# Performance work log

Hardware: AMD Instinct MI355X
Metric: run time of the kernel (lower is better)

The kernel has to match this reference:

```python
import jax, jax.numpy as jnp
import numpy as np

B, A, D, K = 262144, 10, 10, 32  # batch, aspects, aspect dim (=10), projection dim


def setup_inputs() -> dict:
    key = jax.random.key(0)
    ks = jax.random.split(key, 7)
    scale = 0.01
    return {
        "user_rep": jax.random.normal(ks[0], (B, A, D), jnp.float32),
        "item_rep": jax.random.normal(ks[1], (B, A, D), jnp.float32),
        "affinity_matrix": jax.random.uniform(ks[2], (D, D), jnp.float32, -scale, scale),
        "user_projection": jax.random.uniform(ks[3], (K, D), jnp.float32, -scale, scale),
        "user_parameters": jax.random.uniform(ks[4], (K, 1), jnp.float32, -scale, scale),
        "item_projection": jax.random.uniform(ks[5], (K, D), jnp.float32, -scale, scale),
        "item_parameters": jax.random.uniform(ks[6], (K, 1), jnp.float32, -scale, scale),
    }


def reference(user_rep, item_rep, affinity_matrix, user_projection,
              user_parameters, item_projection, item_parameters):
    # affinity: relu( U @ M @ V^T )  -> [B, Au, Av]
    aff = jax.nn.relu(jnp.einsum('bud,de,bve->buv', user_rep, affinity_matrix, item_rep))

    h_user = jnp.einsum('kd,bud->bku', user_projection, user_rep)  # [B,K,Au]
    h_item = jnp.einsum('kd,bvd->bkv', item_projection, item_rep)  # [B,K,Av]

    # user importance branch
    hu = jax.nn.relu(h_user + jnp.einsum('bkv,buv->bku', h_item, aff))
    u_score = jnp.einsum('k,bku->bu', user_parameters[:, 0], hu)   # [B,Au]
    user_asp_importance = jax.nn.softmax(u_score, axis=1)

    # item importance branch
    hi = jax.nn.relu(h_item + jnp.einsum('bku,buv->bkv', h_user, aff))
    i_score = jnp.einsum('k,bkv->bv', item_parameters[:, 0], hi)   # [B,Av]
    item_asp_importance = jax.nn.softmax(i_score, axis=1)

    return (user_asp_importance, item_asp_importance)
```

## Files before the change

kernel.cpp:

```cpp
#include <hip/hip_runtime.h>

#define NB 262144
#define AA 10
#define DD 10
#define KK 32

typedef float v2f __attribute__((ext_vector_type(2)));

static __device__ __forceinline__ float b2f(unsigned short h) {
    union { unsigned u; float f; } c; c.u = ((unsigned)h) << 16; return c.f;
}
static __device__ __forceinline__ float bflo(unsigned w) {
    union { unsigned u; float f; } c; c.u = w << 16; return c.f;
}
static __device__ __forceinline__ float bfhi(unsigned w) {
    union { unsigned u; float f; } c; c.u = w & 0xffff0000u; return c.f;
}
static __device__ __forceinline__ v2f mk2(float a, float b) {
    v2f r; r.x = a; r.y = b; return r;
}

__device__ __forceinline__ int detect_f32(const unsigned short* p, int nshorts,
                                          unsigned expthr, int lane) {
    int bad = 0;
    if (lane < nshorts) {
        unsigned e = (p[lane] >> 7) & 0xFFu;
        bad = (e >= expthr);
    }
    return __any(bad);
}

__global__ __launch_bounds__(64) void prep_weights(
    const unsigned short* __restrict__ wM,
    const unsigned short* __restrict__ wPu,
    const unsigned short* __restrict__ wpu,
    const unsigned short* __restrict__ wPi,
    const unsigned short* __restrict__ wpi,
    float* __restrict__ wf)
{
    const int t = threadIdx.x;
    int f = 0;
    f |= detect_f32(wM,  64, 125, t) << 0;
    f |= detect_f32(wPu, 64, 125, t) << 1;
    f |= detect_f32(wpu, 32, 125, t) << 2;
    f |= detect_f32(wPi, 64, 125, t) << 3;
    f |= detect_f32(wpi, 32, 125, t) << 4;
    const float* fM  = (const float*)wM;
    const float* fPu = (const float*)wPu;
    const float* fpu = (const float*)wpu;
    const float* fPi = (const float*)wPi;
    const float* fpi = (const float*)wpi;
    for (int i = t; i < 100; i += 64) wf[i]       = (f & 1)  ? fM[i]  : b2f(wM[i]);
    for (int i = t; i < 320; i += 64) wf[100 + i] = (f & 2)  ? fPu[i] : b2f(wPu[i]);
    if (t < 32)                       wf[420 + t] = (f & 4)  ? fpu[t] : b2f(wpu[t]);
    for (int i = t; i < 320; i += 64) wf[452 + i] = (f & 8)  ? fPi[i] : b2f(wPi[i]);
    if (t < 32)                       wf[772 + t] = (f & 16) ? fpi[t] : b2f(wpi[t]);
}

__global__ __launch_bounds__(64, 2) void aie_main(
    const unsigned short* __restrict__ user_rep,
    const unsigned short* __restrict__ item_rep,
    const float* __restrict__ wf,
    float* __restrict__ out)
{
    __shared__ float obuf[1408];
    const int t = threadIdx.x;
    const long long b = (long long)blockIdx.x * 64 + t;

    const int fu = detect_f32(user_rep, 64, 137, t);
    const int fi = detect_f32(item_rep, 64, 137, t);

    v2f U2[AA][5], V2[AA][5];

    if (fi) {
        const float4* g = (const float4*)((const float*)item_rep + b * 100);
        #pragma unroll
        for (int j = 0; j < 25; j++) {
            float4 w = g[j];
            int p = 2 * j;
            V2[p / 5][p % 5]             = mk2(w.x, w.y);
            V2[(p + 1) / 5][(p + 1) % 5] = mk2(w.z, w.w);
        }
    } else {
        const uint2* g = (const uint2*)(item_rep + b * 100);
        #pragma unroll
        for (int j = 0; j < 25; j++) {
            uint2 w = g[j];
            int p = 2 * j;
            V2[p / 5][p % 5]             = mk2(bflo(w.x), bfhi(w.x));
            V2[(p + 1) / 5][(p + 1) % 5] = mk2(bflo(w.y), bfhi(w.y));
        }
    }
    if (fu) {
        const float4* g = (const float4*)((const float*)user_rep + b * 100);
        #pragma unroll
        for (int j = 0; j < 25; j++) {
            float4 w = g[j];
            int p = 2 * j;
            U2[p / 5][p % 5]             = mk2(w.x, w.y);
            U2[(p + 1) / 5][(p + 1) % 5] = mk2(w.z, w.w);
        }
    } else {
        const uint2* g = (const uint2*)(user_rep + b * 100);
        #pragma unroll
        for (int j = 0; j < 25; j++) {
            uint2 w = g[j];
            int p = 2 * j;
            U2[p / 5][p % 5]             = mk2(bflo(w.x), bfhi(w.x));
            U2[(p + 1) / 5][(p + 1) % 5] = mk2(bflo(w.y), bfhi(w.y));
        }
    }

    const v2f*  M2  = (const v2f*)wf;
    const v2f*  Pu2 = (const v2f*)(wf + 100);
    const float* pu = wf + 420;
    const v2f*  Pi2 = (const v2f*)(wf + 452);
    const float* pi = wf + 772;

    #pragma unroll
    for (int u = 0; u < AA; u++) {
        v2f um2[5];
        {
            const float x0 = U2[u][0].x;
            #pragma unroll
            for (int j = 0; j < 5; j++) um2[j] = x0 * M2[j];
        }
        #pragma unroll
        for (int d = 1; d < DD; d++) {
            const float x = (d & 1) ? U2[u][d >> 1].y : U2[u][d >> 1].x;
            #pragma unroll
            for (int j = 0; j < 5; j++) um2[j] += x * M2[d * 5 + j];
        }
        v2f Wr2[5];
        #pragma unroll
        for (int j = 0; j < 5; j++) Wr2[j] = mk2(0.f, 0.f);
        #pragma unroll
        for (int v = 0; v < AA; v++) {
            v2f r2 = um2[0] * V2[v][0];
            #pragma unroll
            for (int j = 1; j < 5; j++) r2 += um2[j] * V2[v][j];
            const float r = fmaxf(r2.x + r2.y, 0.f);
            #pragma unroll
            for (int j = 0; j < 5; j++) Wr2[j] += r * V2[v][j];
        }
        float acc = 0.f;
        #pragma unroll 1
        for (int k0 = 0; k0 < KK; k0 += 8) {
            #pragma unroll
            for (int kk = 0; kk < 8; kk++) {
                const int k = k0 + kk;
                v2f a2 = Pu2[k * 5] * U2[u][0];
                v2f c2 = Pi2[k * 5] * Wr2[0];
                #pragma unroll
                for (int j = 1; j < 5; j++) {
                    a2 += Pu2[k * 5 + j] * U2[u][j];
                    c2 += Pi2[k * 5 + j] * Wr2[j];
                }
                const v2f s2 = a2 + c2;
                acc += pu[k] * fmaxf(s2.x + s2.y, 0.f);
            }
        }
        obuf[11 * t + u] = acc;
    }

    #pragma unroll
    for (int v = 0; v < AA; v++) {
        v2f mv2[5];
        #pragma unroll
        for (int dp = 0; dp < 5; dp++) {
            v2f s0 = M2[(2 * dp) * 5]     * V2[v][0];
            v2f s1 = M2[(2 * dp + 1) * 5] * V2[v][0];
            #pragma unroll
            for (int j = 1; j < 5; j++) {
                s0 += M2[(2 * dp) * 5 + j]     * V2[v][j];
                s1 += M2[(2 * dp + 1) * 5 + j] * V2[v][j];
            }
            mv2[dp] = mk2(s0.x + s0.y, s1.x + s1.y);
        }
        v2f Xr2[5];
        #pragma unroll
        for (int j = 0; j < 5; j++) Xr2[j] = mk2(0.f, 0.f);
        #pragma unroll
        for (int u = 0; u < AA; u++) {
            v2f r2 = mv2[0] * U2[u][0];
            #pragma unroll
            for (int j = 1; j < 5; j++) r2 += mv2[j] * U2[u][j];
            const float r = fmaxf(r2.x + r2.y, 0.f);
            #pragma unroll
            for (int j = 0; j < 5; j++) Xr2[j] += r * U2[u][j];
        }
        float acc = 0.f;
        #pragma unroll 1
        for (int k0 = 0; k0 < KK; k0 += 8) {
            #pragma unroll
            for (int kk = 0; kk < 8; kk++) {
                const int k = k0 + kk;
                v2f a2 = Pi2[k * 5] * V2[v][0];
                v2f c2 = Pu2[k * 5] * Xr2[0];
                #pragma unroll
                for (int j = 1; j < 5; j++) {
                    a2 += Pi2[k * 5 + j] * V2[v][j];
                    c2 += Pu2[k * 5 + j] * Xr2[j];
                }
                const v2f s2 = a2 + c2;
                acc += pi[k] * fmaxf(s2.x + s2.y, 0.f);
            }
        }
        obuf[704 + 11 * t + v] = acc;
    }

    #pragma unroll
    for (int h = 0; h < 2; h++) {
        const int base = 704 * h + 11 * t;
        float s[AA];
        #pragma unroll
        for (int u = 0; u < AA; u++) s[u] = obuf[base + u];
        float mx = s[0];
        #pragma unroll
        for (int u = 1; u < AA; u++) mx = fmaxf(mx, s[u]);
        float sum = 0.f;
        #pragma unroll
        for (int u = 0; u < AA; u++) { s[u] = __expf(s[u] - mx); sum += s[u]; }
        const float inv = 1.f / sum;
        #pragma unroll
        for (int u = 0; u < AA; u++) obuf[base + u] = s[u] * inv;
    }
    __syncthreads();

    {
        float2* o0 = (float2*)(out + (size_t)blockIdx.x * 640);
        float2* o1 = (float2*)(out + (size_t)NB * 10 + (size_t)blockIdx.x * 640);
        #pragma unroll
        for (int j = 0; j < 5; j++) {
            int m = t + 64 * j;
            int i = m / 5;
            int u = 2 * (m - 5 * i);
            o0[m] = make_float2(obuf[11 * i + u],       obuf[11 * i + u + 1]);
            o1[m] = make_float2(obuf[704 + 11 * i + u], obuf[704 + 11 * i + u + 1]);
        }
    }
}

extern "C" void kernel_launch(void* const* d_in, const int* in_sizes, int n_in,
                              void* d_out, int out_size, void* d_ws, size_t ws_size,
                              hipStream_t stream) {
    const unsigned short* user_rep = (const unsigned short*)d_in[0];
    const unsigned short* item_rep = (const unsigned short*)d_in[1];
    float* wf = (float*)d_ws;

    hipLaunchKernelGGL(prep_weights, dim3(1), dim3(64), 0, stream,
                       (const unsigned short*)d_in[2], (const unsigned short*)d_in[3],
                       (const unsigned short*)d_in[4], (const unsigned short*)d_in[5],
                       (const unsigned short*)d_in[6], wf);

    hipLaunchKernelGGL(aie_main, dim3(NB / 64), dim3(64), 0, stream,
                       user_rep, item_rep, wf, (float*)d_out);
}
```

Before: 320.1 us.

## Interchange projection loops to k-outer with packed FMA and LDS-stashed intermediates

Restructures both importance branches so the K projection loop is outermost and loops over all 10 aspects inside it. Each k's interleaved weight row is then loaded once, as a uniform scalar operand, and reused across aspects. Weights are repacked in the prep kernel into per-k 24-float rows, and the arithmetic is written as inline-asm v_pk_fma/v_pk_mul with SGPR operands. The affinity-weighted vectors are stashed in per-thread LDS and item_rep is reloaded from global to limit register pressure. Outputs are written directly per thread, which drops the shared-memory transpose and __syncthreads but gives less coalesced stores and adds an extra global read.

```diff
diff --git a/kernel.cpp b/kernel.cpp
--- a/kernel.cpp
+++ b/kernel.cpp
@@ -7,6 +7,25 @@
 
 typedef float v2f __attribute__((ext_vector_type(2)));
 
+static __device__ __forceinline__ v2f mk2(float a, float b) {
+    v2f r; r.x = a; r.y = b; return r;
+}
+static __device__ __forceinline__ v2f pk_fma(v2f a, v2f b, v2f c) {
+    v2f d; asm("v_pk_fma_f32 %0, %1, %2, %3" : "=v"(d) : "v"(a), "v"(b), "v"(c)); return d;
+}
+static __device__ __forceinline__ v2f pk_fma_s(v2f sa, v2f b, v2f c) {
+    v2f d; asm("v_pk_fma_f32 %0, %1, %2, %3" : "=v"(d) : "s"(sa), "v"(b), "v"(c)); return d;
+}
+static __device__ __forceinline__ v2f pk_mul(v2f a, v2f b) {
+    v2f d; asm("v_pk_mul_f32 %0, %1, %2" : "=v"(d) : "v"(a), "v"(b)); return d;
+}
+static __device__ __forceinline__ v2f pk_mul_s(v2f sa, v2f b) {
+    v2f d; asm("v_pk_mul_f32 %0, %1, %2" : "=v"(d) : "s"(sa), "v"(b)); return d;
+}
+static __device__ __forceinline__ v2f pk_add(v2f a, v2f b) {
+    v2f d; asm("v_pk_add_f32 %0, %1, %2" : "=v"(d) : "v"(a), "v"(b)); return d;
+}
+
 static __device__ __forceinline__ float b2f(unsigned short h) {
     union { unsigned u; float f; } c; c.u = ((unsigned)h) << 16; return c.f;
 }
@@ -15,9 +34,6 @@
 }
 static __device__ __forceinline__ float bfhi(unsigned w) {
     union { unsigned u; float f; } c; c.u = w & 0xffff0000u; return c.f;
-}
-static __device__ __forceinline__ v2f mk2(float a, float b) {
-    v2f r; r.x = a; r.y = b; return r;
 }
 
 __device__ __forceinline__ int detect_f32(const unsigned short* p, int nshorts,
@@ -50,11 +66,48 @@
     const float* fpu = (const float*)wpu;
     const float* fPi = (const float*)wPi;
     const float* fpi = (const float*)wpi;
-    for (int i = t; i < 100; i += 64) wf[i]       = (f & 1)  ? fM[i]  : b2f(wM[i]);
-    for (int i = t; i < 320; i += 64) wf[100 + i] = (f & 2)  ? fPu[i] : b2f(wPu[i]);
-    if (t < 32)                       wf[420 + t] = (f & 4)  ? fpu[t] : b2f(wpu[t]);
-    for (int i = t; i < 320; i += 64) wf[452 + i] = (f & 8)  ? fPi[i] : b2f(wPi[i]);
-    if (t < 32)                       wf[772 + t] = (f & 16) ? fpi[t] : b2f(wpi[t]);
+
+    for (int i = t; i < 100; i += 64) wf[i] = (f & 1) ? fM[i] : b2f(wM[i]);
+
+    for (int i = t; i < KK * 24; i += 64) {
+        const int k = i / 24, j = i % 24;
+        float vu = 0.f, vi = 0.f;
+        if (j < 10) {
+            vu = (f & 2) ? fPu[k * 10 + j] : b2f(wPu[k * 10 + j]);
+            vi = (f & 8) ? fPi[k * 10 + j] : b2f(wPi[k * 10 + j]);
+        } else if (j < 20) {
+            vu = (f & 8) ? fPi[k * 10 + j - 10] : b2f(wPi[k * 10 + j - 10]);
+            vi = (f & 2) ? fPu[k * 10 + j - 10] : b2f(wPu[k * 10 + j - 10]);
+        } else if (j == 20) {
+            vu = (f & 4)  ? fpu[k] : b2f(wpu[k]);
+            vi = (f & 16) ? fpi[k] : b2f(wpi[k]);
+        }
+        wf[128 + i] = vu;
+        wf[896 + i] = vi;
+    }
+}
+
+static __device__ __forceinline__ void load_rep(const unsigned short* __restrict__ p,
+                                                int isf32, long long b, v2f R[AA][5]) {
+    if (isf32) {
+        const float4* g = (const float4*)((const float*)p + b * 100);
+        #pragma unroll
+        for (int j = 0; j < 25; j++) {
+            float4 w = g[j];
+            int e = 2 * j;
+            R[e / 5][e % 5]             = mk2(w.x, w.y);
+            R[(e + 1) / 5][(e + 1) % 5] = mk2(w.z, w.w);
+        }
+    } else {
+        const uint2* g = (const uint2*)(p + b * 100);
+        #pragma unroll
+        for (int j = 0; j < 25; j++) {
+            uint2 w = g[j];
+            int e = 2 * j;
+            R[e / 5][e % 5]             = mk2(bflo(w.x), bfhi(w.x));
+            R[(e + 1) / 5][(e + 1) % 5] = mk2(bflo(w.y), bfhi(w.y));
+        }
+    }
 }
 
 __global__ __launch_bounds__(64, 2) void aie_main(
@@ -63,181 +116,167 @@
     const float* __restrict__ wf,
     float* __restrict__ out)
 {
-    __shared__ float obuf[1408];
+    __shared__ v2f stash[64 * 51];
     const int t = threadIdx.x;
     const long long b = (long long)blockIdx.x * 64 + t;
+    v2f* my = &stash[t * 51];
 
     const int fu = detect_f32(user_rep, 64, 137, t);
     const int fi = detect_f32(item_rep, 64, 137, t);
 
     v2f U2[AA][5], V2[AA][5];
-
-    if (fi) {
-        const float4* g = (const float4*)((const float*)item_rep + b * 100);
-        #pragma unroll
-        for (int j = 0; j < 25; j++) {
-            float4 w = g[j];
-            int p = 2 * j;
-            V2[p / 5][p % 5]             = mk2(w.x, w.y);
-            V2[(p + 1) / 5][(p + 1) % 5] = mk2(w.z, w.w);
-        }
-    } else {
-        const uint2* g = (const uint2*)(item_rep + b * 100);
-        #pragma unroll
-        for (int j = 0; j < 25; j++) {
-            uint2 w = g[j];
-            int p = 2 * j;
-            V2[p / 5][p % 5]             = mk2(bflo(w.x), bfhi(w.x));
-            V2[(p + 1) / 5][(p + 1) % 5] = mk2(bflo(w.y), bfhi(w.y));
-        }
-    }
-    if (fu) {
-        const float4* g = (const float4*)((const float*)user_rep + b * 100);
-        #pragma unroll
-        for (int j = 0; j < 25; j++) {
-            float4 w = g[j];
-            int p = 2 * j;
-            U2[p / 5][p % 5]             = mk2(w.x, w.y);
-            U2[(p + 1) / 5][(p + 1) % 5] = mk2(w.z, w.w);
-        }
-    } else {
-        const uint2* g = (const uint2*)(user_rep + b * 100);
-        #pragma unroll
-        for (int j = 0; j < 25; j++) {
-            uint2 w = g[j];
-            int p = 2 * j;
-            U2[p / 5][p % 5]             = mk2(bflo(w.x), bfhi(w.x));
-            U2[(p + 1) / 5][(p + 1) % 5] = mk2(bflo(w.y), bfhi(w.y));
-        }
-    }
-
-    const v2f*  M2  = (const v2f*)wf;
-    const v2f*  Pu2 = (const v2f*)(wf + 100);
-    const float* pu = wf + 420;
-    const v2f*  Pi2 = (const v2f*)(wf + 452);
-    const float* pi = wf + 772;
+    load_rep(item_rep, fi, b, V2);
+    load_rep(user_rep, fu, b, U2);
+
+    const v2f* M2 = (const v2f*)wf;
 
     #pragma unroll
     for (int u = 0; u < AA; u++) {
         v2f um2[5];
         {
-            const float x0 = U2[u][0].x;
-            #pragma unroll
-            for (int j = 0; j < 5; j++) um2[j] = x0 * M2[j];
+            v2f xs = mk2(U2[u][0].x, U2[u][0].x);
+            #pragma unroll
+            for (int j = 0; j < 5; j++) um2[j] = pk_mul_s(M2[j], xs);
         }
         #pragma unroll
         for (int d = 1; d < DD; d++) {
             const float x = (d & 1) ? U2[u][d >> 1].y : U2[u][d >> 1].x;
-            #pragma unroll
-            for (int j = 0; j < 5; j++) um2[j] += x * M2[d * 5 + j];
-        }
-        v2f Wr2[5];
-        #pragma unroll
-        for (int j = 0; j < 5; j++) Wr2[j] = mk2(0.f, 0.f);
+            v2f xs = mk2(x, x);
+            #pragma unroll
+            for (int j = 0; j < 5; j++) um2[j] = pk_fma_s(M2[d * 5 + j], xs, um2[j]);
+        }
+        v2f Wr[5];
+        #pragma unroll
+        for (int j = 0; j < 5; j++) Wr[j] = mk2(0.f, 0.f);
         #pragma unroll
         for (int v = 0; v < AA; v++) {
-            v2f r2 = um2[0] * V2[v][0];
-            #pragma unroll
-            for (int j = 1; j < 5; j++) r2 += um2[j] * V2[v][j];
+            v2f r2 = pk_mul(um2[0], V2[v][0]);
+            #pragma unroll
+            for (int j = 1; j < 5; j++) r2 = pk_fma(um2[j], V2[v][j], r2);
             const float r = fmaxf(r2.x + r2.y, 0.f);
-            #pragma unroll
-            for (int j = 0; j < 5; j++) Wr2[j] += r * V2[v][j];
-        }
-        float acc = 0.f;
-        #pragma unroll 1
-        for (int k0 = 0; k0 < KK; k0 += 8) {
-            #pragma unroll
-            for (int kk = 0; kk < 8; kk++) {
-                const int k = k0 + kk;
-                v2f a2 = Pu2[k * 5] * U2[u][0];
-                v2f c2 = Pi2[k * 5] * Wr2[0];
-                #pragma unroll
-                for (int j = 1; j < 5; j++) {
-                    a2 += Pu2[k * 5 + j] * U2[u][j];
-                    c2 += Pi2[k * 5 + j] * Wr2[j];
-                }
-                const v2f s2 = a2 + c2;
-                acc += pu[k] * fmaxf(s2.x + s2.y, 0.f);
+            v2f rs = mk2(r, r);
+            #pragma unroll
+            for (int j = 0; j < 5; j++) Wr[j] = pk_fma(rs, V2[v][j], Wr[j]);
+        }
+        #pragma unroll
+        for (int j = 0; j < 5; j++) my[u * 5 + j] = Wr[j];
+    }
+    asm volatile("" ::: "memory");
+
+    v2f Wf[AA][5];
+    #pragma unroll
+    for (int u = 0; u < AA; u++)
+        #pragma unroll
+        for (int j = 0; j < 5; j++) Wf[u][j] = my[u * 5 + j];
+
+    float us[AA];
+    #pragma unroll
+    for (int u = 0; u < AA; u++) us[u] = 0.f;
+    #pragma unroll 2
+    for (int k = 0; k < KK; k++) {
+        const v2f* wk = (const v2f*)(wf + 128 + k * 24);
+        const float pw = wf[128 + k * 24 + 20];
+        #pragma unroll
+        for (int u = 0; u < AA; u++) {
+            v2f a2 = pk_mul_s(wk[0], U2[u][0]);
+            v2f c2 = pk_mul_s(wk[5], Wf[u][0]);
+            #pragma unroll
+            for (int j = 1; j < 5; j++) {
+                a2 = pk_fma_s(wk[j],     U2[u][j], a2);
+                c2 = pk_fma_s(wk[5 + j], Wf[u][j], c2);
             }
-        }
-        obuf[11 * t + u] = acc;
-    }
+            v2f s2 = pk_add(a2, c2);
+            us[u] += pw * fmaxf(s2.x + s2.y, 0.f);
+        }
+    }
+
+    {
+        float mx = us[0];
+        #pragma unroll
+        for (int u = 1; u < AA; u++) mx = fmaxf(mx, us[u]);
+        float s = 0.f;
+        #pragma unroll
+        for (int u = 0; u < AA; u++) { us[u] = __expf(us[u] - mx); s += us[u]; }
+        const float inv = 1.f / s;
+        float* o0 = out + b * 10;
+        #pragma unroll
+        for (int j = 0; j < 5; j++)
+            *(float2*)(o0 + 2 * j) = make_float2(us[2 * j] * inv, us[2 * j + 1] * inv);
+    }
+
+    load_rep(item_rep, fi, b, V2);
 
     #pragma unroll
     for (int v = 0; v < AA; v++) {
         v2f mv2[5];
         #pragma unroll
         for (int dp = 0; dp < 5; dp++) {
-            v2f s0 = M2[(2 * dp) * 5]     * V2[v][0];
-            v2f s1 = M2[(2 * dp + 1) * 5] * V2[v][0];
+            v2f s0 = pk_mul_s(M2[(2 * dp) * 5],     V2[v][0]);
+            v2f s1 = pk_mul_s(M2[(2 * dp + 1) * 5], V2[v][0]);
             #pragma unroll
             for (int j = 1; j < 5; j++) {
-                s0 += M2[(2 * dp) * 5 + j]     * V2[v][j];
-                s1 += M2[(2 * dp + 1) * 5 + j] * V2[v][j];
+                s0 = pk_fma_s(M2[(2 * dp) * 5 + j],     V2[v][j], s0);
+                s1 = pk_fma_s(M2[(2 * dp + 1) * 5 + j], V2[v][j], s1);
             }
             mv2[dp] = mk2(s0.x + s0.y, s1.x + s1.y);
         }
-        v2f Xr2[5];
-        #pragma unroll
-        for (int j = 0; j < 5; j++) Xr2[j] = mk2(0.f, 0.f);
+        v2f Xr[5];
+        #pragma unroll
+        for (int j = 0; j < 5; j++) Xr[j] = mk2(0.f, 0.f);
         #pragma unroll
         for (int u = 0; u < AA; u++) {
-            v2f r2 = mv2[0] * U2[u][0];
-            #pragma unroll
-            for (int j = 1; j < 5; j++) r2 += mv2[j] * U2[u][j];
+            v2f r2 = pk_mul(mv2[0], U2[u][0]);
+            #pragma unroll
+            for (int j = 1; j < 5; j++) r2 = pk_fma(mv2[j], U2[u][j], r2);
             const float r = fmaxf(r2.x + r2.y, 0.f);
-            #pragma unroll
-            for (int j = 0; j < 5; j++) Xr2[j] += r * U2[u][j];
-        }
-        float acc = 0.f;
-        #pragma unroll 1
-        for (int k0 = 0; k0 < KK; k0 += 8) {
-            #pragma unroll
-            for (int kk = 0; kk < 8; kk++) {
-                const int k = k0 + kk;
-                v2f a2 = Pi2[k * 5] * V2[v][0];
-                v2f c2 = Pu2[k * 5] * Xr2[0];
-                #pragma unroll
-                for (int j = 1; j < 5; j++) {
-                    a2 += Pi2[k * 5 + j] * V2[v][j];
-                    c2 += Pu2[k * 5 + j] * Xr2[j];
-                }
-                const v2f s2 = a2 + c2;
-                acc += pi[k] * fmaxf(s2.x + s2.y, 0.f);
+            v2f rs = mk2(r, r);
+            #pragma unroll
+            for (int j = 0; j < 5; j++) Xr[j] = pk_fma(rs, U2[u][j], Xr[j]);
+        }
+        #pragma unroll
+        for (int j = 0; j < 5; j++) my[v * 5 + j] = Xr[j];
+    }
+    asm volatile("" ::: "memory");
+
+    v2f Xf[AA][5];
+    #pragma unroll
+    for (int v = 0; v < AA; v++)
+        #pragma unroll
+        for (int j = 0; j < 5; j++) Xf[v][j] = my[v * 5 + j];
+
+    float isc[AA];
+    #pragma unroll
+    for (int v = 0; v < AA; v++) isc[v] = 0.f;
+    #pragma unroll 2
+    for (int k = 0; k < KK; k++) {
+        const v2f* wk = (const v2f*)(wf + 896 + k * 24);
+        const float pw = wf[896 + k * 24 + 20];
+        #pragma unroll
+        for (int v = 0; v < AA; v++) {
+            v2f a2 = pk_mul_s(wk[0], V2[v][0]);
+            v2f c2 = pk_mul_s(wk[5], Xf[v][0]);
+            #pragma unroll
+            for (int j = 1; j < 5; j++) {
+                a2 = pk_fma_s(wk[j],     V2[v][j], a2);
+                c2 = pk_fma_s(wk[5 + j], Xf[v][j], c2);
             }
-        }
-        obuf[704 + 11 * t + v] = acc;
-    }
-
-    #pragma unroll
-    for (int h = 0; h < 2; h++) {
-        const int base = 704 * h + 11 * t;
-        float s[AA];
-        #pragma unroll
-        for (int u = 0; u < AA; u++) s[u] = obuf[base + u];
-        float mx = s[0];
-        #pragma unroll
-        for (int u = 1; u < AA; u++) mx = fmaxf(mx, s[u]);
-        float sum = 0.f;
-        #pragma unroll
-        for (int u = 0; u < AA; u++) { s[u] = __expf(s[u] - mx); sum += s[u]; }
-        const float inv = 1.f / sum;
-        #pragma unroll
-        for (int u = 0; u < AA; u++) obuf[base + u] = s[u] * inv;
-    }
-    __syncthreads();
+            v2f s2 = pk_add(a2, c2);
+            isc[v] += pw * fmaxf(s2.x + s2.y, 0.f);
+        }
+    }
 
     {
-        float2* o0 = (float2*)(out + (size_t)blockIdx.x * 640);
-        float2* o1 = (float2*)(out + (size_t)NB * 10 + (size_t)blockIdx.x * 640);
-        #pragma unroll
-        for (int j = 0; j < 5; j++) {
-            int m = t + 64 * j;
-            int i = m / 5;
-            int u = 2 * (m - 5 * i);
-            o0[m] = make_float2(obuf[11 * i + u],       obuf[11 * i + u + 1]);
-            o1[m] = make_float2(obuf[704 + 11 * i + u], obuf[704 + 11 * i + u + 1]);
-        }
+        float mx = isc[0];
+        #pragma unroll
+        for (int v = 1; v < AA; v++) mx = fmaxf(mx, isc[v]);
+        float s = 0.f;
+        #pragma unroll
+        for (int v = 0; v < AA; v++) { isc[v] = __expf(isc[v] - mx); s += isc[v]; }
+        const float inv = 1.f / s;
+        float* o1 = out + (size_t)NB * 10 + b * 10;
+        #pragma unroll
+        for (int j = 0; j < 5; j++)
+            *(float2*)(o1 + 2 * j) = make_float2(isc[2 * j] * inv, isc[2 * j + 1] * inv);
     }
 }
 
```

Measured after the change: 374.2 us. 1.17x slower.
